# Performance work log

Measured on AMD Instinct MI355X. Metric: run time of the kernel, lower is better.

The kernel has to match this reference:

```python
import jax, jax.numpy as jnp
import numpy as np

# geomloss SamplesLoss(loss='sinkhorn', p=2, reach=1.0, blur=0.1) constants
P = 2
BLUR = 0.1
REACH = 1.0
SCALING = 0.5
EPS_FINAL = BLUR ** P          # 0.01
RHO = REACH ** P               # 1.0
DIAMETER = 2.0 * np.sqrt(2.0)  # PMT positions scaled to [-1,1]^2


def eps_schedule():
    # geomloss epsilon_schedule(p, diameter, blur, scaling)
    e = [DIAMETER ** P]
    for t in np.arange(P * np.log(DIAMETER), P * np.log(BLUR), P * np.log(SCALING)):
        e.append(float(np.exp(t)))
    e.append(BLUR ** P)
    return [float(v) for v in e]


def _softmin(eps, C, h):
    # h: (B, N) log-measure + potential/eps ; C: (N, N) shared cost -> (B, N)
    return -eps * jax.scipy.special.logsumexp(h[:, None, :] - C[None, :, :] / eps, axis=-1)


def _sinkhorn_potentials(a_log, b_log, C):
    # symmetric unbalanced Sinkhorn loop with eps-annealing (geomloss sinkhorn_loop)
    eps_list = eps_schedule()
    damp = lambda eps: 1.0 / (1.0 + eps / RHO)
    eps0 = eps_list[0]
    d0 = damp(eps0)
    g_ab = d0 * _softmin(eps0, C, a_log)
    f_ba = d0 * _softmin(eps0, C, b_log)
    f_aa = d0 * _softmin(eps0, C, a_log)
    g_bb = d0 * _softmin(eps0, C, b_log)
    for eps in eps_list:
        d = damp(eps)
        ft = d * _softmin(eps, C, b_log + g_ab / eps)
        gt = d * _softmin(eps, C, a_log + f_ba / eps)
        f_ba, g_ab = 0.5 * (f_ba + ft), 0.5 * (g_ab + gt)
        f_aa = 0.5 * (f_aa + d * _softmin(eps, C, a_log + f_aa / eps))
        g_bb = 0.5 * (g_bb + d * _softmin(eps, C, b_log + g_bb / eps))
    # last extrapolation at the final (target) temperature
    eps = eps_list[-1]
    d = damp(eps)
    f_ba, g_ab = (d * _softmin(eps, C, b_log + g_ab / eps),
                  d * _softmin(eps, C, a_log + f_ba / eps))
    f_aa = d * _softmin(eps, C, a_log + f_aa / eps)
    g_bb = d * _softmin(eps, C, b_log + g_bb / eps)
    return f_aa, g_bb, g_ab, f_ba


def setup_inputs() -> dict:
    key = jax.random.key(0)
    k1, k2, k3 = jax.random.split(key, 3)
    B, N = 32768, 32
    # positive PE weights (measure masses must be > 0 for log-domain Sinkhorn)
    pred_pmtpe = jax.random.uniform(k1, (B, N), jnp.float32, 0.05, 1.0)
    target_pe = jax.random.uniform(k2, (B, N), jnp.float32, 0.05, 1.0)
    # fixed scaled 2D (z,y) PMT layout in [-1,1]^2, shared by pred and target clouds
    pmt_pos = jax.random.uniform(k3, (N, 2), jnp.float32, -1.0, 1.0)
    batchstart = jnp.arange(B, dtype=jnp.int64) * N
    batchend = batchstart + N
    return {"pred_pmtpe": pred_pmtpe, "target_pe": target_pe, "pmt_pos": pmt_pos,
            "batchstart": batchstart, "batchend": batchend}


def reference(pred_pmtpe, target_pe, pmt_pos, batchstart, batchend):
    # shared cost matrix (x_pred_batch == y_target_batch == PMT layout), C = |x-y|^2/2 for p=2
    C = 0.5 * jnp.sum((pmt_pos[:, None, :] - pmt_pos[None, :, :]) ** 2, axis=-1)  # (32,32)
    # geomloss runs the Sinkhorn loop with autograd disabled (envelope theorem)
    a_log = jnp.log(jax.lax.stop_gradient(pred_pmtpe))
    b_log = jnp.log(jax.lax.stop_gradient(target_pe))
    f_aa, g_bb, g_ab, f_ba = _sinkhorn_potentials(a_log, b_log, C)
    f_aa, g_bb, g_ab, f_ba = map(jax.lax.stop_gradient, (f_aa, g_bb, g_ab, f_ba))
    # unbalanced debiased sinkhorn cost (geomloss sinkhorn_cost, rho finite)
    eps = EPS_FINAL
    scale = RHO + 0.5 * eps
    per_batch = scale * (
        jnp.sum(pred_pmtpe * (jnp.exp(-f_aa / RHO) - jnp.exp(-f_ba / RHO)), axis=-1)
        + jnp.sum(target_pe * (jnp.exp(-g_bb / RHO) - jnp.exp(-g_ab / RHO)), axis=-1)
    )
    return jnp.mean(per_batch)
```

## Files before the change

### kernel.cpp

```cpp
#include <hip/hip_runtime.h>

#define EXP2F(x)  __builtin_amdgcn_exp2f(x)
#define LOG2FD(x) __builtin_amdgcn_logf(x)
#define L2E 1.4426950408889634f
#define T1F 1.2621774e-29f

typedef __attribute__((ext_vector_type(8))) short bf16x8;
typedef __attribute__((ext_vector_type(4))) float f32x4;
typedef __attribute__((ext_vector_type(2))) unsigned int u32x2;

#define MFMA16(A, B, C) __builtin_amdgcn_mfma_f32_16x16x32_bf16((A), (B), (C), 0, 0, 0)

union U8 { unsigned int u[4]; bf16x8 v; };

__device__ __forceinline__ void split_pack(const float* w, bf16x8& hi, bf16x8& lo) {
  U8 a, b;
#pragma unroll
  for (int k = 0; k < 4; ++k) {
    float x0 = w[2*k], x1 = w[2*k+1];
    unsigned u0 = __float_as_uint(x0) & 0xFFFF0000u;
    unsigned u1 = __float_as_uint(x1) & 0xFFFF0000u;
    float r0 = x0 - __uint_as_float(u0);
    float r1 = x1 - __uint_as_float(u1);
    a.u[k] = (u0 >> 16) | u1;
    b.u[k] = ((__float_as_uint(r0) & 0xFFFF0000u) >> 16) |
             (__float_as_uint(r1) & 0xFFFF0000u);
  }
  hi = a.v; lo = b.v;
}

__device__ __forceinline__ float pmax32(float v) {
  u32x2 r = __builtin_amdgcn_permlane32_swap(__float_as_uint(v), __float_as_uint(v),
                                             false, false);
  return fmaxf(__uint_as_float(r.x), __uint_as_float(r.y));
}

__device__ __forceinline__ void buildK(const float* c2a, const float* c2b, float inv,
                                       bf16x8& KA1, bf16x8& KA2, bf16x8& KB1, bf16x8& KB2) {
  float ka[8], kb[8];
#pragma unroll
  for (int e = 0; e < 8; ++e) { ka[e] = EXP2F(-c2a[e] * inv); kb[e] = EXP2F(-c2b[e] * inv); }
  split_pack(ka, KA1, KA2);
  split_pack(kb, KB1, KB2);
}

__device__ __forceinline__ void pot_assign(float* pot, const float* Ts, int b15, int g) {
  float4 r0 = *(const float4*)&Ts[b15*36 + 8*g];
  float4 r1 = *(const float4*)&Ts[b15*36 + 8*g + 4];
  pot[0]=r0.x; pot[1]=r0.y; pot[2]=r0.z; pot[3]=r0.w;
  pot[4]=r1.x; pot[5]=r1.y; pot[6]=r1.z; pot[7]=r1.w;
}

__device__ __forceinline__ void pot_merge(float* pot, const float* Ts, int b15, int g) {
  float4 r0 = *(const float4*)&Ts[b15*36 + 8*g];
  float4 r1 = *(const float4*)&Ts[b15*36 + 8*g + 4];
  pot[0]=0.5f*(pot[0]+r0.x); pot[1]=0.5f*(pot[1]+r0.y);
  pot[2]=0.5f*(pot[2]+r0.z); pot[3]=0.5f*(pot[3]+r0.w);
  pot[4]=0.5f*(pot[4]+r1.x); pot[5]=0.5f*(pot[5]+r1.y);
  pot[6]=0.5f*(pot[6]+r1.z); pot[7]=0.5f*(pot[7]+r1.w);
}

__device__ __noinline__ float exact_lse(const float2* pos2, const float* HB,
                                        int i, float inv) {
  float2 pi = pos2[i];
  float m = -3.4e38f;
#pragma unroll 1
  for (int j = 0; j < 32; ++j) {
    float2 pj = pos2[j];
    float dx = pi.x - pj.x, dy = pi.y - pj.y;
    float arg = fmaf((0.5f*L2E)*(dx*dx + dy*dy), -inv, HB[j]);
    m = fmaxf(m, arg);
  }
  float s = 0.f;
#pragma unroll 1
  for (int j = 0; j < 32; ++j) {
    float2 pj = pos2[j];
    float dx = pi.x - pj.x, dy = pi.y - pj.y;
    float arg = fmaf((0.5f*L2E)*(dx*dx + dy*dy), -inv, HB[j]);
    s += EXP2F(arg - m);
  }
  return m + LOG2FD(s);
}

template<int NQ, bool CHECKED>
__device__ __forceinline__ void ksoft_multi(float* Ts, float* Hdump,
    const float Hq[][8], bf16x8 KA1, bf16x8 KA2, bf16x8 KB1, bf16x8 KB2,
    float nde, float inv, int b15, int g, const float2* pos2) {
  float hm[NQ], d[NQ][8];
  bf16x8 w1[NQ], w2[NQ];
#pragma unroll
  for (int q = 0; q < NQ; ++q) {
    const float* H = Hq[q];
    float m = fmaxf(fmaxf(fmaxf(H[0], H[1]), fmaxf(H[2], H[3])),
                    fmaxf(fmaxf(H[4], H[5]), fmaxf(H[6], H[7])));
    m = fmaxf(m, __shfl_xor(m, 16));
    m = pmax32(m);
    hm[q] = m;
    float w[8];
#pragma unroll
    for (int e = 0; e < 8; ++e) { d[q][e] = H[e] - m; w[e] = EXP2F(d[q][e]); }
    split_pack(w, w1[q], w2[q]);
  }
  f32x4 a0[NQ], a1[NQ];
  const f32x4 z = {0.f, 0.f, 0.f, 0.f};
#pragma unroll
  for (int q = 0; q < NQ; ++q) { a0[q] = MFMA16(KA1, w1[q], z);     a1[q] = MFMA16(KB1, w1[q], z); }
#pragma unroll
  for (int q = 0; q < NQ; ++q) { a0[q] = MFMA16(KA2, w1[q], a0[q]); a1[q] = MFMA16(KB2, w1[q], a1[q]); }
#pragma unroll
  for (int q = 0; q < NQ; ++q) { a0[q] = MFMA16(KA1, w2[q], a0[q]); a1[q] = MFMA16(KB1, w2[q], a1[q]); }
#pragma unroll
  for (int q = 0; q < NQ; ++q) {
    float r0[4], r1[4];
#pragma unroll
    for (int r = 0; r < 4; ++r) {
      r0[r] = hm[q] + LOG2FD(a0[q][r]);
      r1[r] = hm[q] + LOG2FD(a1[q][r]);
    }
    if (CHECKED) {
      float mn = fminf(fminf(fminf(a0[q][0], a0[q][1]), fminf(a0[q][2], a0[q][3])),
                       fminf(fminf(a1[q][0], a1[q][1]), fminf(a1[q][2], a1[q][3])));
      if (__any(mn < T1F)) {
        float wb[8];
#pragma unroll
        for (int e = 0; e < 8; ++e) wb[e] = EXP2F(d[q][e] + 96.f);
        bf16x8 u1, u2;
        split_pack(wb, u1, u2);
        f32x4 b0 = MFMA16(KA1, u1, z);
        b0 = MFMA16(KA2, u1, b0);
        b0 = MFMA16(KA1, u2, b0);
        f32x4 b1 = MFMA16(KB1, u1, z);
        b1 = MFMA16(KB2, u1, b1);
        b1 = MFMA16(KB1, u2, b1);
        bool mybad = false;
#pragma unroll
        for (int r = 0; r < 4; ++r) {
          if (a0[q][r] < T1F) r0[r] = (hm[q] - 96.f) + LOG2FD(b0[r]);
          if (a1[q][r] < T1F) r1[r] = (hm[q] - 96.f) + LOG2FD(b1[r]);
          mybad |= (a0[q][r] < T1F) && (b0[r] < T1F);
          mybad |= (a1[q][r] < T1F) && (b1[r] < T1F);
        }
        if (__any(mybad)) {
          float4 h0 = {Hq[q][0], Hq[q][1], Hq[q][2], Hq[q][3]};
          float4 h1 = {Hq[q][4], Hq[q][5], Hq[q][6], Hq[q][7]};
          *(float4*)&Hdump[b15*36 + 8*g]     = h0;
          *(float4*)&Hdump[b15*36 + 8*g + 4] = h1;
          asm volatile("" ::: "memory");
          const float* HB = &Hdump[b15*36];
#pragma unroll
          for (int r = 0; r < 4; ++r) {
            if ((a0[q][r] < T1F) && (b0[r] < T1F)) r0[r] = exact_lse(pos2, HB, 4*g + r, inv);
            if ((a1[q][r] < T1F) && (b1[r] < T1F)) r1[r] = exact_lse(pos2, HB, 16 + 4*g + r, inv);
          }
        }
      }
    }
    float4 v0 = {nde*r0[0], nde*r0[1], nde*r0[2], nde*r0[3]};
    float4 v1 = {nde*r1[0], nde*r1[1], nde*r1[2], nde*r1[3]};
    float* Tq = Ts + q * 576;
    *(float4*)&Tq[b15*36 + 4*g]      = v0;
    *(float4*)&Tq[b15*36 + 4*g + 16] = v1;
  }
}

__global__ __launch_bounds__(64, 2) void sink_kernel(
    const float* __restrict__ pred, const float* __restrict__ tgt,
    const float* __restrict__ pos, float* __restrict__ ws) {
  __shared__ __align__(16) float sT[4][576];
  __shared__ __align__(16) float sHb[16][36];

  const int lid = threadIdx.x;
  const int b15 = lid & 15;
  const int g   = lid >> 4;
  const int bbase = blockIdx.x * 16;
  const float2* pos2 = (const float2*)pos;
  float* Tw = &sT[0][0];
  float* Hd = &sHb[0][0];

  float al2[8], bl2[8];
  {
    const float* pr = &pred[(bbase + b15) * 32 + 8 * g];
    const float* tr = &tgt [(bbase + b15) * 32 + 8 * g];
    float4 p0 = *(const float4*)&pr[0];
    float4 p1 = *(const float4*)&pr[4];
    float4 t0 = *(const float4*)&tr[0];
    float4 t1 = *(const float4*)&tr[4];
    al2[0]=LOG2FD(p0.x); al2[1]=LOG2FD(p0.y); al2[2]=LOG2FD(p0.z); al2[3]=LOG2FD(p0.w);
    al2[4]=LOG2FD(p1.x); al2[5]=LOG2FD(p1.y); al2[6]=LOG2FD(p1.z); al2[7]=LOG2FD(p1.w);
    bl2[0]=LOG2FD(t0.x); bl2[1]=LOG2FD(t0.y); bl2[2]=LOG2FD(t0.z); bl2[3]=LOG2FD(t0.w);
    bl2[4]=LOG2FD(t1.x); bl2[5]=LOG2FD(t1.y); bl2[6]=LOG2FD(t1.z); bl2[7]=LOG2FD(t1.w);
  }
  float c2a[8], c2b[8];
  {
    float2 pm0 = pos2[b15];
    float2 pm1 = pos2[b15 + 16];
#pragma unroll
    for (int e = 0; e < 8; ++e) {
      float2 pj = pos2[8*g + e];
      float dx0 = pm0.x - pj.x, dy0 = pm0.y - pj.y;
      float dx1 = pm1.x - pj.x, dy1 = pm1.y - pj.y;
      c2a[e] = (0.5f*L2E)*(dx0*dx0 + dy0*dy0);
      c2b[e] = (0.5f*L2E)*(dx1*dx1 + dy1*dy1);
    }
  }

  bf16x8 KA1, KA2, KB1, KB2;
  float Fba[8], Gab[8], Faa[8], Gbb[8];

  buildK(c2a, c2b, 0.125f, KA1, KA2, KB1, KB2);
  {
    float Hq[2][8];
#pragma unroll
    for (int e = 0; e < 8; ++e) { Hq[0][e] = bl2[e]; Hq[1][e] = al2[e]; }
    ksoft_multi<2, false>(Tw, Hd, Hq, KA1, KA2, KB1, KB2, -8.f/9.f, 0.125f, b15, g, pos2);
  }
  pot_assign(Fba, Tw + 0*576, b15, g);
  pot_assign(Gab, Tw + 1*576, b15, g);
#pragma unroll
  for (int e = 0; e < 8; ++e) { Faa[e] = Gab[e]; Gbb[e] = Fba[e]; }

  const float INV[8] = {0.125f, 0.125f, 0.5f, 2.f, 8.f, 32.f, 100.f, 100.f};
  const float NDE[8] = {-8.f/9.f, -8.f/9.f, -2.f/3.f, -1.f/3.f, -1.f/9.f,
                        -1.f/33.f, -1.f/101.f, -1.f/101.f};
  float curInv = 0.125f;

#pragma unroll 1
  for (int k = 0; k < 5; ++k) {
    const float inv = INV[k], nde = NDE[k];
    if (inv != curInv) { buildK(c2a, c2b, inv, KA1, KA2, KB1, KB2); curInv = inv; }
    float Hq[4][8];
#pragma unroll
    for (int e = 0; e < 8; ++e) {
      Hq[0][e] = fmaf(Gab[e], inv, bl2[e]);
      Hq[1][e] = fmaf(Fba[e], inv, al2[e]);
      Hq[2][e] = fmaf(Faa[e], inv, al2[e]);
      Hq[3][e] = fmaf(Gbb[e], inv, bl2[e]);
    }
    ksoft_multi<4, false>(Tw, Hd, Hq, KA1, KA2, KB1, KB2, nde, inv, b15, g, pos2);
    pot_merge(Fba, Tw + 0*576, b15, g);
    pot_merge(Gab, Tw + 1*576, b15, g);
    pot_merge(Faa, Tw + 2*576, b15, g);
    pot_merge(Gbb, Tw + 3*576, b15, g);
  }

#pragma unroll 1
  for (int k = 5; k < 8; ++k) {
    const float inv = INV[k], nde = NDE[k];
    if (inv != curInv) { buildK(c2a, c2b, inv, KA1, KA2, KB1, KB2); curInv = inv; }
    const bool avg = (k < 7);
    float Hq[4][8];
#pragma unroll
    for (int e = 0; e < 8; ++e) {
      Hq[0][e] = fmaf(Gab[e], inv, bl2[e]);
      Hq[1][e] = fmaf(Fba[e], inv, al2[e]);
      Hq[2][e] = fmaf(Faa[e], inv, al2[e]);
      Hq[3][e] = fmaf(Gbb[e], inv, bl2[e]);
    }
    ksoft_multi<4, true>(Tw, Hd, Hq, KA1, KA2, KB1, KB2, nde, inv, b15, g, pos2);
    if (avg) {
      pot_merge(Fba, Tw + 0*576, b15, g);
      pot_merge(Gab, Tw + 1*576, b15, g);
      pot_merge(Faa, Tw + 2*576, b15, g);
      pot_merge(Gbb, Tw + 3*576, b15, g);
    } else {
      pot_assign(Fba, Tw + 0*576, b15, g);
      pot_assign(Gab, Tw + 1*576, b15, g);
      pot_assign(Faa, Tw + 2*576, b15, g);
      pot_assign(Gbb, Tw + 3*576, b15, g);
    }
  }

  float c = 0.f;
#pragma unroll
  for (int e = 0; e < 8; ++e) {
    c += EXP2F(al2[e]) * (EXP2F(-Faa[e]) - EXP2F(-Fba[e]))
       + EXP2F(bl2[e]) * (EXP2F(-Gbb[e]) - EXP2F(-Gab[e]));
  }
  c += __shfl_xor(c, 1);
  c += __shfl_xor(c, 2);
  c += __shfl_xor(c, 4);
  c += __shfl_xor(c, 8);
  c += __shfl_xor(c, 16);
  c += __shfl_xor(c, 32);
  if (lid == 0) ws[blockIdx.x] = c;
}

__global__ __launch_bounds__(256) void reduce_kernel(
    const float* __restrict__ ws, float* __restrict__ out, int n, float scale) {
  float s = 0.f;
  for (int i = threadIdx.x; i < n; i += 256) s += ws[i];
  s += __shfl_xor(s, 32);
  s += __shfl_xor(s, 16);
  s += __shfl_xor(s, 8);
  s += __shfl_xor(s, 4);
  s += __shfl_xor(s, 2);
  s += __shfl_xor(s, 1);
  __shared__ float a[4];
  if ((threadIdx.x & 63) == 0) a[threadIdx.x >> 6] = s;
  __syncthreads();
  if (threadIdx.x == 0) out[0] = ((a[0] + a[1]) + (a[2] + a[3])) * scale;
}

extern "C" void kernel_launch(void* const* d_in, const int* in_sizes, int n_in,
                              void* d_out, int out_size, void* d_ws, size_t ws_size,
                              hipStream_t stream) {
  const float* pred = (const float*)d_in[0];
  const float* tgt  = (const float*)d_in[1];
  const float* pos  = (const float*)d_in[2];
  const int B = in_sizes[0] / 32;
  const int nblocks = B / 16;
  float* ws = (float*)d_ws;

  sink_kernel<<<nblocks, 64, 0, stream>>>(pred, tgt, pos, ws);
  reduce_kernel<<<1, 256, 0, stream>>>(ws, (float*)d_out, nblocks,
                                       1.005f / (float)B);
}
```

Measured before the change: 28.97 us.

## Split batch work across MFMA columns to halve per-wave softmin count

Each wave now processes 8 batches instead of 16. The 16 MFMA columns are arranged so that one half of the columns carries the pred-side potentials and the other half the target-side ones, which cuts each iteration from four softmin queries to two. Cross potentials are exchanged through the shared-memory tile by reading the partner column (b15^8). The cost matrix is recomputed from positions inside buildK instead of being kept in registers. Per-block LDS shrinks and launch bounds rise to 4 waves per SIMD for higher occupancy, in exchange for twice as many blocks and some redundant position loads.

```diff
diff --git a/kernel.cpp b/kernel.cpp
--- a/kernel.cpp
+++ b/kernel.cpp
@@ -35,29 +35,22 @@
   return fmaxf(__uint_as_float(r.x), __uint_as_float(r.y));
 }
 
-__device__ __forceinline__ void buildK(const float* c2a, const float* c2b, float inv,
+__device__ __forceinline__ void buildK(const float2* pos2, float inv,
+                                       int b15, int g,
                                        bf16x8& KA1, bf16x8& KA2, bf16x8& KB1, bf16x8& KB2) {
+  float2 p0 = pos2[b15];
+  float2 p1 = pos2[b15 + 16];
   float ka[8], kb[8];
 #pragma unroll
-  for (int e = 0; e < 8; ++e) { ka[e] = EXP2F(-c2a[e] * inv); kb[e] = EXP2F(-c2b[e] * inv); }
+  for (int e = 0; e < 8; ++e) {
+    float2 pj = pos2[8*g + e];
+    float dx0 = p0.x - pj.x, dy0 = p0.y - pj.y;
+    float dx1 = p1.x - pj.x, dy1 = p1.y - pj.y;
+    ka[e] = EXP2F((-0.5f*L2E) * inv * (dx0*dx0 + dy0*dy0));
+    kb[e] = EXP2F((-0.5f*L2E) * inv * (dx1*dx1 + dy1*dy1));
+  }
   split_pack(ka, KA1, KA2);
   split_pack(kb, KB1, KB2);
-}
-
-__device__ __forceinline__ void pot_assign(float* pot, const float* Ts, int b15, int g) {
-  float4 r0 = *(const float4*)&Ts[b15*36 + 8*g];
-  float4 r1 = *(const float4*)&Ts[b15*36 + 8*g + 4];
-  pot[0]=r0.x; pot[1]=r0.y; pot[2]=r0.z; pot[3]=r0.w;
-  pot[4]=r1.x; pot[5]=r1.y; pot[6]=r1.z; pot[7]=r1.w;
-}
-
-__device__ __forceinline__ void pot_merge(float* pot, const float* Ts, int b15, int g) {
-  float4 r0 = *(const float4*)&Ts[b15*36 + 8*g];
-  float4 r1 = *(const float4*)&Ts[b15*36 + 8*g + 4];
-  pot[0]=0.5f*(pot[0]+r0.x); pot[1]=0.5f*(pot[1]+r0.y);
-  pot[2]=0.5f*(pot[2]+r0.z); pot[3]=0.5f*(pot[3]+r0.w);
-  pot[4]=0.5f*(pot[4]+r1.x); pot[5]=0.5f*(pot[5]+r1.y);
-  pot[6]=0.5f*(pot[6]+r1.z); pot[7]=0.5f*(pot[7]+r1.w);
 }
 
 __device__ __noinline__ float exact_lse(const float2* pos2, const float* HB,
@@ -82,15 +75,17 @@
   return m + LOG2FD(s);
 }
 
-template<int NQ, bool CHECKED>
-__device__ __forceinline__ void ksoft_multi(float* Ts, float* Hdump,
-    const float Hq[][8], bf16x8 KA1, bf16x8 KA2, bf16x8 KB1, bf16x8 KB2,
+template<bool CHECKED>
+__device__ __forceinline__ void ksoft2(float* Ts, float* Hdump,
+    float* H1, float* H2,
+    bf16x8 KA1, bf16x8 KA2, bf16x8 KB1, bf16x8 KB2,
     float nde, float inv, int b15, int g, const float2* pos2) {
-  float hm[NQ], d[NQ][8];
-  bf16x8 w1[NQ], w2[NQ];
-#pragma unroll
-  for (int q = 0; q < NQ; ++q) {
-    const float* H = Hq[q];
+  float* Hq[2] = {H1, H2};
+  float hm[2];
+  bf16x8 w1[2], w2[2];
+#pragma unroll
+  for (int q = 0; q < 2; ++q) {
+    float* H = Hq[q];
     float m = fmaxf(fmaxf(fmaxf(H[0], H[1]), fmaxf(H[2], H[3])),
                     fmaxf(fmaxf(H[4], H[5]), fmaxf(H[6], H[7])));
     m = fmaxf(m, __shfl_xor(m, 16));
@@ -98,19 +93,20 @@
     hm[q] = m;
     float w[8];
 #pragma unroll
-    for (int e = 0; e < 8; ++e) { d[q][e] = H[e] - m; w[e] = EXP2F(d[q][e]); }
+    for (int e = 0; e < 8; ++e) { H[e] -= m; w[e] = EXP2F(H[e]); }
     split_pack(w, w1[q], w2[q]);
   }
-  f32x4 a0[NQ], a1[NQ];
   const f32x4 z = {0.f, 0.f, 0.f, 0.f};
-#pragma unroll
-  for (int q = 0; q < NQ; ++q) { a0[q] = MFMA16(KA1, w1[q], z);     a1[q] = MFMA16(KB1, w1[q], z); }
-#pragma unroll
-  for (int q = 0; q < NQ; ++q) { a0[q] = MFMA16(KA2, w1[q], a0[q]); a1[q] = MFMA16(KB2, w1[q], a1[q]); }
-#pragma unroll
-  for (int q = 0; q < NQ; ++q) { a0[q] = MFMA16(KA1, w2[q], a0[q]); a1[q] = MFMA16(KB1, w2[q], a1[q]); }
-#pragma unroll
-  for (int q = 0; q < NQ; ++q) {
+  f32x4 a0[2], a1[2];
+#pragma unroll
+  for (int q = 0; q < 2; ++q) { a0[q] = MFMA16(KA1, w1[q], z);     a1[q] = MFMA16(KB1, w1[q], z); }
+#pragma unroll
+  for (int q = 0; q < 2; ++q) { a0[q] = MFMA16(KA2, w1[q], a0[q]); a1[q] = MFMA16(KB2, w1[q], a1[q]); }
+#pragma unroll
+  for (int q = 0; q < 2; ++q) { a0[q] = MFMA16(KA1, w2[q], a0[q]); a1[q] = MFMA16(KB1, w2[q], a1[q]); }
+#pragma unroll
+  for (int q = 0; q < 2; ++q) {
+    float* H = Hq[q];
     float r0[4], r1[4];
 #pragma unroll
     for (int r = 0; r < 4; ++r) {
@@ -123,7 +119,7 @@
       if (__any(mn < T1F)) {
         float wb[8];
 #pragma unroll
-        for (int e = 0; e < 8; ++e) wb[e] = EXP2F(d[q][e] + 96.f);
+        for (int e = 0; e < 8; ++e) wb[e] = EXP2F(H[e] + 96.f);
         bf16x8 u1, u2;
         split_pack(wb, u1, u2);
         f32x4 b0 = MFMA16(KA1, u1, z);
@@ -141,8 +137,8 @@
           mybad |= (a1[q][r] < T1F) && (b1[r] < T1F);
         }
         if (__any(mybad)) {
-          float4 h0 = {Hq[q][0], Hq[q][1], Hq[q][2], Hq[q][3]};
-          float4 h1 = {Hq[q][4], Hq[q][5], Hq[q][6], Hq[q][7]};
+          float4 h0 = {H[0]+hm[q], H[1]+hm[q], H[2]+hm[q], H[3]+hm[q]};
+          float4 h1 = {H[4]+hm[q], H[5]+hm[q], H[6]+hm[q], H[7]+hm[q]};
           *(float4*)&Hdump[b15*36 + 8*g]     = h0;
           *(float4*)&Hdump[b15*36 + 8*g + 4] = h1;
           asm volatile("" ::: "memory");
@@ -163,61 +159,65 @@
   }
 }
 
-__global__ __launch_bounds__(64, 2) void sink_kernel(
+__global__ __launch_bounds__(64, 4) void sink_kernel(
     const float* __restrict__ pred, const float* __restrict__ tgt,
     const float* __restrict__ pos, float* __restrict__ ws) {
-  __shared__ __align__(16) float sT[4][576];
-  __shared__ __align__(16) float sHb[16][36];
-
-  const int lid = threadIdx.x;
-  const int b15 = lid & 15;
-  const int g   = lid >> 4;
-  const int bbase = blockIdx.x * 16;
+  __shared__ __align__(16) float sT[2][576];
+  __shared__ __align__(16) float sHb[16 * 36];
+
+  const int lid  = threadIdx.x;
+  const int b15  = lid & 15;
+  const int g    = lid >> 4;
+  const int h8   = (b15 >> 3) & 1;
+  const int bcol = b15 & 7;
+  const int bbase = blockIdx.x * 8;
   const float2* pos2 = (const float2*)pos;
   float* Tw = &sT[0][0];
-  float* Hd = &sHb[0][0];
-
-  float al2[8], bl2[8];
+  float* Hd = &sHb[0];
+
+  float m1[8], m2[8];
   {
-    const float* pr = &pred[(bbase + b15) * 32 + 8 * g];
-    const float* tr = &tgt [(bbase + b15) * 32 + 8 * g];
+    const float* pr = &pred[(bbase + bcol) * 32 + 8 * g];
+    const float* tr = &tgt [(bbase + bcol) * 32 + 8 * g];
     float4 p0 = *(const float4*)&pr[0];
     float4 p1 = *(const float4*)&pr[4];
     float4 t0 = *(const float4*)&tr[0];
     float4 t1 = *(const float4*)&tr[4];
-    al2[0]=LOG2FD(p0.x); al2[1]=LOG2FD(p0.y); al2[2]=LOG2FD(p0.z); al2[3]=LOG2FD(p0.w);
-    al2[4]=LOG2FD(p1.x); al2[5]=LOG2FD(p1.y); al2[6]=LOG2FD(p1.z); al2[7]=LOG2FD(p1.w);
-    bl2[0]=LOG2FD(t0.x); bl2[1]=LOG2FD(t0.y); bl2[2]=LOG2FD(t0.z); bl2[3]=LOG2FD(t0.w);
-    bl2[4]=LOG2FD(t1.x); bl2[5]=LOG2FD(t1.y); bl2[6]=LOG2FD(t1.z); bl2[7]=LOG2FD(t1.w);
-  }
-  float c2a[8], c2b[8];
+    float la[8], lb[8];
+    la[0]=LOG2FD(p0.x); la[1]=LOG2FD(p0.y); la[2]=LOG2FD(p0.z); la[3]=LOG2FD(p0.w);
+    la[4]=LOG2FD(p1.x); la[5]=LOG2FD(p1.y); la[6]=LOG2FD(p1.z); la[7]=LOG2FD(p1.w);
+    lb[0]=LOG2FD(t0.x); lb[1]=LOG2FD(t0.y); lb[2]=LOG2FD(t0.z); lb[3]=LOG2FD(t0.w);
+    lb[4]=LOG2FD(t1.x); lb[5]=LOG2FD(t1.y); lb[6]=LOG2FD(t1.z); lb[7]=LOG2FD(t1.w);
+#pragma unroll
+    for (int e = 0; e < 8; ++e) {
+      m1[e] = h8 ? la[e] : lb[e];
+      m2[e] = h8 ? lb[e] : la[e];
+    }
+  }
+
+  bf16x8 KA1, KA2, KB1, KB2;
+  float Xo[8], Xc[8], W[8];
+  float H1[8], H2[8];
+
+  buildK(pos2, 0.125f, b15, g, KA1, KA2, KB1, KB2);
+#pragma unroll
+  for (int e = 0; e < 8; ++e) { H1[e] = m1[e]; H2[e] = m2[e]; }
+  ksoft2<false>(Tw, Hd, H1, H2, KA1, KA2, KB1, KB2, -8.f/9.f, 0.125f, b15, g, pos2);
   {
-    float2 pm0 = pos2[b15];
-    float2 pm1 = pos2[b15 + 16];
-#pragma unroll
-    for (int e = 0; e < 8; ++e) {
-      float2 pj = pos2[8*g + e];
-      float dx0 = pm0.x - pj.x, dy0 = pm0.y - pj.y;
-      float dx1 = pm1.x - pj.x, dy1 = pm1.y - pj.y;
-      c2a[e] = (0.5f*L2E)*(dx0*dx0 + dy0*dy0);
-      c2b[e] = (0.5f*L2E)*(dx1*dx1 + dy1*dy1);
-    }
-  }
-
-  bf16x8 KA1, KA2, KB1, KB2;
-  float Fba[8], Gab[8], Faa[8], Gbb[8];
-
-  buildK(c2a, c2b, 0.125f, KA1, KA2, KB1, KB2);
-  {
-    float Hq[2][8];
-#pragma unroll
-    for (int e = 0; e < 8; ++e) { Hq[0][e] = bl2[e]; Hq[1][e] = al2[e]; }
-    ksoft_multi<2, false>(Tw, Hd, Hq, KA1, KA2, KB1, KB2, -8.f/9.f, 0.125f, b15, g, pos2);
-  }
-  pot_assign(Fba, Tw + 0*576, b15, g);
-  pot_assign(Gab, Tw + 1*576, b15, g);
-#pragma unroll
-  for (int e = 0; e < 8; ++e) { Faa[e] = Gab[e]; Gbb[e] = Fba[e]; }
+    const int own = b15 * 36 + 8 * g, crs = (b15 ^ 8) * 36 + 8 * g;
+    float4 o0 = *(const float4*)&Tw[own];
+    float4 o1 = *(const float4*)&Tw[own + 4];
+    float4 c0 = *(const float4*)&Tw[crs];
+    float4 c1 = *(const float4*)&Tw[crs + 4];
+    float4 s0 = *(const float4*)&Tw[576 + own];
+    float4 s1 = *(const float4*)&Tw[576 + own + 4];
+    Xo[0]=o0.x; Xo[1]=o0.y; Xo[2]=o0.z; Xo[3]=o0.w;
+    Xo[4]=o1.x; Xo[5]=o1.y; Xo[6]=o1.z; Xo[7]=o1.w;
+    Xc[0]=c0.x; Xc[1]=c0.y; Xc[2]=c0.z; Xc[3]=c0.w;
+    Xc[4]=c1.x; Xc[5]=c1.y; Xc[6]=c1.z; Xc[7]=c1.w;
+    W[0]=s0.x;  W[1]=s0.y;  W[2]=s0.z;  W[3]=s0.w;
+    W[4]=s1.x;  W[5]=s1.y;  W[6]=s1.z;  W[7]=s1.w;
+  }
 
   const float INV[8] = {0.125f, 0.125f, 0.5f, 2.f, 8.f, 32.f, 100.f, 100.f};
   const float NDE[8] = {-8.f/9.f, -8.f/9.f, -2.f/3.f, -1.f/3.f, -1.f/9.f,
@@ -227,62 +227,72 @@
 #pragma unroll 1
   for (int k = 0; k < 5; ++k) {
     const float inv = INV[k], nde = NDE[k];
-    if (inv != curInv) { buildK(c2a, c2b, inv, KA1, KA2, KB1, KB2); curInv = inv; }
-    float Hq[4][8];
+    if (inv != curInv) { buildK(pos2, inv, b15, g, KA1, KA2, KB1, KB2); curInv = inv; }
 #pragma unroll
     for (int e = 0; e < 8; ++e) {
-      Hq[0][e] = fmaf(Gab[e], inv, bl2[e]);
-      Hq[1][e] = fmaf(Fba[e], inv, al2[e]);
-      Hq[2][e] = fmaf(Faa[e], inv, al2[e]);
-      Hq[3][e] = fmaf(Gbb[e], inv, bl2[e]);
-    }
-    ksoft_multi<4, false>(Tw, Hd, Hq, KA1, KA2, KB1, KB2, nde, inv, b15, g, pos2);
-    pot_merge(Fba, Tw + 0*576, b15, g);
-    pot_merge(Gab, Tw + 1*576, b15, g);
-    pot_merge(Faa, Tw + 2*576, b15, g);
-    pot_merge(Gbb, Tw + 3*576, b15, g);
+      H1[e] = fmaf(Xc[e], inv, m1[e]);
+      H2[e] = fmaf(W[e],  inv, m2[e]);
+    }
+    ksoft2<false>(Tw, Hd, H1, H2, KA1, KA2, KB1, KB2, nde, inv, b15, g, pos2);
+    const int own = b15 * 36 + 8 * g, crs = (b15 ^ 8) * 36 + 8 * g;
+    float4 o0 = *(const float4*)&Tw[own];
+    float4 o1 = *(const float4*)&Tw[own + 4];
+    float4 c0 = *(const float4*)&Tw[crs];
+    float4 c1 = *(const float4*)&Tw[crs + 4];
+    float4 s0 = *(const float4*)&Tw[576 + own];
+    float4 s1 = *(const float4*)&Tw[576 + own + 4];
+    Xo[0]=0.5f*(Xo[0]+o0.x); Xo[1]=0.5f*(Xo[1]+o0.y); Xo[2]=0.5f*(Xo[2]+o0.z); Xo[3]=0.5f*(Xo[3]+o0.w);
+    Xo[4]=0.5f*(Xo[4]+o1.x); Xo[5]=0.5f*(Xo[5]+o1.y); Xo[6]=0.5f*(Xo[6]+o1.z); Xo[7]=0.5f*(Xo[7]+o1.w);
+    Xc[0]=0.5f*(Xc[0]+c0.x); Xc[1]=0.5f*(Xc[1]+c0.y); Xc[2]=0.5f*(Xc[2]+c0.z); Xc[3]=0.5f*(Xc[3]+c0.w);
+    Xc[4]=0.5f*(Xc[4]+c1.x); Xc[5]=0.5f*(Xc[5]+c1.y); Xc[6]=0.5f*(Xc[6]+c1.z); Xc[7]=0.5f*(Xc[7]+c1.w);
+    W[0]=0.5f*(W[0]+s0.x);  W[1]=0.5f*(W[1]+s0.y);  W[2]=0.5f*(W[2]+s0.z);  W[3]=0.5f*(W[3]+s0.w);
+    W[4]=0.5f*(W[4]+s1.x);  W[5]=0.5f*(W[5]+s1.y);  W[6]=0.5f*(W[6]+s1.z);  W[7]=0.5f*(W[7]+s1.w);
   }
 
 #pragma unroll 1
   for (int k = 5; k < 8; ++k) {
     const float inv = INV[k], nde = NDE[k];
-    if (inv != curInv) { buildK(c2a, c2b, inv, KA1, KA2, KB1, KB2); curInv = inv; }
-    const bool avg = (k < 7);
-    float Hq[4][8];
+    if (inv != curInv) { buildK(pos2, inv, b15, g, KA1, KA2, KB1, KB2); curInv = inv; }
 #pragma unroll
     for (int e = 0; e < 8; ++e) {
-      Hq[0][e] = fmaf(Gab[e], inv, bl2[e]);
-      Hq[1][e] = fmaf(Fba[e], inv, al2[e]);
-      Hq[2][e] = fmaf(Faa[e], inv, al2[e]);
-      Hq[3][e] = fmaf(Gbb[e], inv, bl2[e]);
-    }
-    ksoft_multi<4, true>(Tw, Hd, Hq, KA1, KA2, KB1, KB2, nde, inv, b15, g, pos2);
-    if (avg) {
-      pot_merge(Fba, Tw + 0*576, b15, g);
-      pot_merge(Gab, Tw + 1*576, b15, g);
-      pot_merge(Faa, Tw + 2*576, b15, g);
-      pot_merge(Gbb, Tw + 3*576, b15, g);
+      H1[e] = fmaf(Xc[e], inv, m1[e]);
+      H2[e] = fmaf(W[e],  inv, m2[e]);
+    }
+    ksoft2<true>(Tw, Hd, H1, H2, KA1, KA2, KB1, KB2, nde, inv, b15, g, pos2);
+    const int own = b15 * 36 + 8 * g, crs = (b15 ^ 8) * 36 + 8 * g;
+    float4 o0 = *(const float4*)&Tw[own];
+    float4 o1 = *(const float4*)&Tw[own + 4];
+    float4 c0 = *(const float4*)&Tw[crs];
+    float4 c1 = *(const float4*)&Tw[crs + 4];
+    float4 s0 = *(const float4*)&Tw[576 + own];
+    float4 s1 = *(const float4*)&Tw[576 + own + 4];
+    if (k < 7) {
+      Xo[0]=0.5f*(Xo[0]+o0.x); Xo[1]=0.5f*(Xo[1]+o0.y); Xo[2]=0.5f*(Xo[2]+o0.z); Xo[3]=0.5f*(Xo[3]+o0.w);
+      Xo[4]=0.5f*(Xo[4]+o1.x); Xo[5]=0.5f*(Xo[5]+o1.y); Xo[6]=0.5f*(Xo[6]+o1.z); Xo[7]=0.5f*(Xo[7]+o1.w);
+      Xc[0]=0.5f*(Xc[0]+c0.x); Xc[1]=0.5f*(Xc[1]+c0.y); Xc[2]=0.5f*(Xc[2]+c0.z); Xc[3]=0.5f*(Xc[3]+c0.w);
+      Xc[4]=0.5f*(Xc[4]+c1.x); Xc[5]=0.5f*(Xc[5]+c1.y); Xc[6]=0.5f*(Xc[6]+c1.z); Xc[7]=0.5f*(Xc[7]+c1.w);
+      W[0]=0.5f*(W[0]+s0.x);  W[1]=0.5f*(W[1]+s0.y);  W[2]=0.5f*(W[2]+s0.z);  W[3]=0.5f*(W[3]+s0.w);
+      W[4]=0.5f*(W[4]+s1.x);  W[5]=0.5f*(W[5]+s1.y);  W[6]=0.5f*(W[6]+s1.z);  W[7]=0.5f*(W[7]+s1.w);
     } else {
-      pot_assign(Fba, Tw + 0*576, b15, g);
-      pot_assign(Gab, Tw + 1*576, b15, g);
-      pot_assign(Faa, Tw + 2*576, b15, g);
-      pot_assign(Gbb, Tw + 3*576, b15, g);
-    }
-  }
-
-  float c = 0.f;
-#pragma unroll
-  for (int e = 0; e < 8; ++e) {
-    c += EXP2F(al2[e]) * (EXP2F(-Faa[e]) - EXP2F(-Fba[e]))
-       + EXP2F(bl2[e]) * (EXP2F(-Gbb[e]) - EXP2F(-Gab[e]));
-  }
-  c += __shfl_xor(c, 1);
-  c += __shfl_xor(c, 2);
-  c += __shfl_xor(c, 4);
-  c += __shfl_xor(c, 8);
-  c += __shfl_xor(c, 16);
-  c += __shfl_xor(c, 32);
-  if (lid == 0) ws[blockIdx.x] = c;
+      Xo[0]=o0.x; Xo[1]=o0.y; Xo[2]=o0.z; Xo[3]=o0.w;
+      Xo[4]=o1.x; Xo[5]=o1.y; Xo[6]=o1.z; Xo[7]=o1.w;
+      W[0]=s0.x;  W[1]=s0.y;  W[2]=s0.z;  W[3]=s0.w;
+      W[4]=s1.x;  W[5]=s1.y;  W[6]=s1.z;  W[7]=s1.w;
+    }
+  }
+
+  float part = 0.f;
+#pragma unroll
+  for (int e = 0; e < 8; ++e)
+    part += EXP2F(m2[e]) * (EXP2F(-W[e]) - EXP2F(-Xo[e]));
+
+  part += __shfl_xor(part, 1);
+  part += __shfl_xor(part, 2);
+  part += __shfl_xor(part, 4);
+  part += __shfl_xor(part, 8);
+  part += __shfl_xor(part, 16);
+  part += __shfl_xor(part, 32);
+  if (lid == 0) ws[blockIdx.x] = part;
 }
 
 __global__ __launch_bounds__(256) void reduce_kernel(
@@ -308,7 +318,7 @@
   const float* tgt  = (const float*)d_in[1];
   const float* pos  = (const float*)d_in[2];
   const int B = in_sizes[0] / 32;
-  const int nblocks = B / 16;
+  const int nblocks = B / 8;
   float* ws = (float*)d_ws;
 
   sink_kernel<<<nblocks, 64, 0, stream>>>(pred, tgt, pos, ws);
```

New measurement: 40.27 us. 1.39x slower.
